# Performance work log

Measured on AMD Instinct MI355X. Metric: run time of the kernel, lower is better.

Reference implementation:

```python
import jax, jax.numpy as jnp
import numpy as np

INPUT_SIZE = 1024
OUTPUT_SIZE = 15
EXPERT_NUM = 10
BS = 65536


def setup_inputs() -> dict:
    key = jax.random.key(0)
    k1, k2, k3, k4, k5 = jax.random.split(key, 5)
    bound = 1.0 / np.sqrt(INPUT_SIZE)
    x = jax.random.normal(k1, (BS, INPUT_SIZE), dtype=jnp.float32)
    expert_w = jax.random.uniform(k2, (EXPERT_NUM, OUTPUT_SIZE, INPUT_SIZE), minval=-bound, maxval=bound, dtype=jnp.float32)
    expert_b = jax.random.uniform(k3, (EXPERT_NUM, OUTPUT_SIZE), minval=-bound, maxval=bound, dtype=jnp.float32)
    gate_w = jax.random.uniform(k4, (EXPERT_NUM, OUTPUT_SIZE, INPUT_SIZE), minval=-bound, maxval=bound, dtype=jnp.float32)
    gate_b = jax.random.uniform(k5, (EXPERT_NUM, OUTPUT_SIZE), minval=-bound, maxval=bound, dtype=jnp.float32)
    return {"x": x, "expert_w": expert_w, "expert_b": expert_b, "gate_w": gate_w, "gate_b": gate_b}


def reference(x, expert_w, expert_b, gate_w, gate_b):
    # miu, xi: (bs, out, E) -- matches torch.stack(..., dim=-1)
    miu = jnp.einsum('bi,eoi->boe', x, expert_w) + expert_b.T[None]  # (bs, out, E)
    xi = jnp.einsum('bi,eoi->boe', x, gate_w) + gate_b.T[None]       # (bs, out, E)
    g = jax.nn.softmax(xi, axis=-1)                                  # softmax over experts
    return jnp.sum(g * miu, axis=-1)                                 # (bs, out)
```

## Files before the change

### kernel.cpp

```cpp
#include <hip/hip_runtime.h>

#define KDIM 1024
#define NOUT 15
#define NEXP 10
#define BM   64
#define BK   32
#define NKS  32
#define QPT  20
#define SCOL 305

typedef short bf16x8 __attribute__((ext_vector_type(8)));
typedef float f32x16 __attribute__((ext_vector_type(16)));

__device__ __forceinline__ unsigned f2bf2(float a, float b) {
    unsigned ua = __float_as_uint(a);
    unsigned ub = __float_as_uint(b);
    ua = (ua + 0x7FFFu + ((ua >> 16) & 1u)) >> 16;
    ub = (ub + 0x7FFFu + ((ub >> 16) & 1u)) & 0xFFFF0000u;
    return ua | ub;
}

__device__ __forceinline__ void dma16(const void* g, void* l) {
    __builtin_amdgcn_global_load_lds(
        (const __attribute__((address_space(1))) unsigned int*)g,
        (__attribute__((address_space(3))) unsigned int*)l, 16, 0, 0);
}

__global__ void wconv_kernel(const float* __restrict__ ew,
                             const float* __restrict__ gw,
                             unsigned short* __restrict__ ws)
{
    int U  = blockIdx.x * 256 + threadIdx.x;
    int L  = U & 63;
    int q  = (U >> 6) % QPT;
    int ks = U / (QPT * 64);
    int nt = q >> 1, kt = q & 1;
    int wrow = nt * 32 + (L & 31);
    int wcol = ks * 32 + kt * 16 + (L >> 5) * 8;
    float4 a = {0.f,0.f,0.f,0.f}, b = {0.f,0.f,0.f,0.f};
    if (wrow < 150) {
        a = *(const float4*)(ew + wrow * KDIM + wcol);
        b = *(const float4*)(ew + wrow * KDIM + wcol + 4);
    } else if (wrow < 300) {
        a = *(const float4*)(gw + (wrow - 150) * KDIM + wcol);
        b = *(const float4*)(gw + (wrow - 150) * KDIM + wcol + 4);
    }
    uint4 o;
    o.x = f2bf2(a.x, a.y); o.y = f2bf2(a.z, a.w);
    o.z = f2bf2(b.x, b.y); o.w = f2bf2(b.z, b.w);
    *(uint4*)(ws + (size_t)U * 8) = o;
}

__global__ void __launch_bounds__(256, 3)
moe_kernel(const float* __restrict__ x,
           const unsigned short* __restrict__ wsrc,
           const float* __restrict__ eb,
           const float* __restrict__ gb,
           float* __restrict__ out)
{
    __shared__ union {
        unsigned short wb[2][QPT * 512];
        float ep[32][SCOL];
    } sm;

    const int tid = threadIdx.x;
    const int wv  = tid >> 6;
    const int L   = tid & 63;
    const int mw  = wv >> 1;
    const int nw  = wv & 1;
    const int ln  = L & 31;
    const int lh  = L >> 5;

    const float* xrow = x + ((size_t)blockIdx.x * BM + mw * 32 + ln) * KDIM + lh * 8;

    f32x16 acc[5];
    #pragma unroll
    for (int nt = 0; nt < 5; ++nt)
        #pragma unroll
        for (int r = 0; r < 16; ++r)
            acc[nt][r] = 0.f;

    #pragma unroll
    for (int i = 0; i < 5; ++i) {
        int q = wv * 5 + i;
        dma16(wsrc + ((size_t)q * 64 + L) * 8, &sm.wb[0][q * 512]);
    }
    float4 xa[2][2];
    #pragma unroll
    for (int kt = 0; kt < 2; ++kt) {
        xa[kt][0] = *(const float4*)(xrow + kt * 16);
        xa[kt][1] = *(const float4*)(xrow + kt * 16 + 4);
    }
    __syncthreads();

    #pragma unroll 2
    for (int ks = 0; ks < NKS; ++ks) {
        float4 xn[2][2];
        if (ks + 1 < NKS) {
            #pragma unroll
            for (int kt = 0; kt < 2; ++kt) {
                xn[kt][0] = *(const float4*)(xrow + (ks + 1) * 32 + kt * 16);
                xn[kt][1] = *(const float4*)(xrow + (ks + 1) * 32 + kt * 16 + 4);
            }
            #pragma unroll
            for (int i = 0; i < 5; ++i) {
                int q = wv * 5 + i;
                dma16(wsrc + (((size_t)(ks + 1) * QPT + q) * 64 + L) * 8,
                      &sm.wb[(ks + 1) & 1][q * 512]);
            }
        }

        bf16x8 af[2];
        #pragma unroll
        for (int kt = 0; kt < 2; ++kt) {
            union { unsigned u[4]; bf16x8 v; } pk;
            pk.u[0] = f2bf2(xa[kt][0].x, xa[kt][0].y);
            pk.u[1] = f2bf2(xa[kt][0].z, xa[kt][0].w);
            pk.u[2] = f2bf2(xa[kt][1].x, xa[kt][1].y);
            pk.u[3] = f2bf2(xa[kt][1].z, xa[kt][1].w);
            af[kt] = pk.v;
        }

        const unsigned short* wbuf = sm.wb[ks & 1];
        #pragma unroll
        for (int nt = 0; nt < 5; ++nt) {
            #pragma unroll
            for (int kt = 0; kt < 2; ++kt) {
                int q = (nw * 5 + nt) * 2 + kt;
                bf16x8 bf = *(const bf16x8*)&wbuf[q * 512 + L * 8];
                acc[nt] = __builtin_amdgcn_mfma_f32_32x32x16_bf16(af[kt], bf, acc[nt], 0, 0, 0);
            }
        }
        __syncthreads();

        #pragma unroll
        for (int kt = 0; kt < 2; ++kt) {
            xa[kt][0] = xn[kt][0];
            xa[kt][1] = xn[kt][1];
        }
    }

    #pragma unroll 1
    for (int g = 0; g < 2; ++g) {
        if (mw == g) {
            #pragma unroll
            for (int nt = 0; nt < 5; ++nt) {
                int col = nw * 160 + nt * 32 + ln;
                if (col < 300) {
                    #pragma unroll
                    for (int r = 0; r < 16; ++r)
                        sm.ep[(r & 3) + 8 * (r >> 2) + 4 * lh][col] = acc[nt][r];
                }
            }
        }
        __syncthreads();

        #pragma unroll 1
        for (int t = tid; t < 32 * NOUT; t += 256) {
            int row = t / NOUT, o = t % NOUT;
            float xi[NEXP], miu_v[NEXP];
            float mx = -1e30f;
            #pragma unroll
            for (int e = 0; e < NEXP; ++e) {
                miu_v[e] = sm.ep[row][e * NOUT + o]       + eb[e * NOUT + o];
                xi[e]    = sm.ep[row][150 + e * NOUT + o] + gb[e * NOUT + o];
                mx = fmaxf(mx, xi[e]);
            }
            float s = 0.f, v = 0.f;
            #pragma unroll
            for (int e = 0; e < NEXP; ++e) {
                float g2 = __expf(xi[e] - mx);
                s += g2;
                v += g2 * miu_v[e];
            }
            out[((size_t)blockIdx.x * BM + g * 32 + row) * NOUT + o] = v / s;
        }
        __syncthreads();
    }
}

extern "C" void kernel_launch(void* const* d_in, const int* in_sizes, int n_in,
                              void* d_out, int out_size, void* d_ws, size_t ws_size,
                              hipStream_t stream) {
    const float* x  = (const float*)d_in[0];
    const float* ew = (const float*)d_in[1];
    const float* eb = (const float*)d_in[2];
    const float* gw = (const float*)d_in[3];
    const float* gb = (const float*)d_in[4];
    float* out = (float*)d_out;
    unsigned short* ws = (unsigned short*)d_ws;

    wconv_kernel<<<160, 256, 0, stream>>>(ew, gw, ws);
    moe_kernel<<<65536 / BM, 256, 0, stream>>>(x, ws, eb, gb, out);
}
```

Before: 416.3 us.

## Stage x tile through LDS as bf16 to stop duplicate global loads

Before, each wave loaded its own copy of the x rows, so the two N-waves (nw=0,1) fetched and converted the same rows twice. Now the block loads each x element once with coalesced loads, converts it to bf16 and writes it into a double-buffered padded LDS tile. The MFMA fragments are then read back from LDS. The global prefetch distance also grows to two k-steps. This halves global x traffic and conversion work, but adds LDS writes and reads and raises shared memory use, which may reduce occupancy.

```diff
diff --git a/kernel.cpp b/kernel.cpp
--- a/kernel.cpp
+++ b/kernel.cpp
@@ -4,10 +4,10 @@
 #define NOUT 15
 #define NEXP 10
 #define BM   64
-#define BK   32
 #define NKS  32
 #define QPT  20
 #define SCOL 305
+#define XSTR 36
 
 typedef short bf16x8 __attribute__((ext_vector_type(8)));
 typedef float f32x16 __attribute__((ext_vector_type(16)));
@@ -59,7 +59,10 @@
            float* __restrict__ out)
 {
     __shared__ union {
-        unsigned short wb[2][QPT * 512];
+        struct {
+            unsigned short wb[2][QPT * 512];
+            unsigned short xb[2][64 * XSTR];
+        } k;
         float ep[32][SCOL];
     } sm;
 
@@ -71,7 +74,12 @@
     const int ln  = L & 31;
     const int lh  = L >> 5;
 
-    const float* xrow = x + ((size_t)blockIdx.x * BM + mw * 32 + ln) * KDIM + lh * 8;
+    const int srow = tid >> 2;
+    const int schk = tid & 3;
+    const float* xg = x + ((size_t)blockIdx.x * BM + srow) * KDIM + schk * 8;
+    const int xwo = srow * XSTR + schk * 8;
+
+    const int xfo = (mw * 32 + ln) * XSTR + lh * 8;
 
     f32x16 acc[5];
     #pragma unroll
@@ -83,61 +91,57 @@
     #pragma unroll
     for (int i = 0; i < 5; ++i) {
         int q = wv * 5 + i;
-        dma16(wsrc + ((size_t)q * 64 + L) * 8, &sm.wb[0][q * 512]);
+        dma16(wsrc + ((size_t)q * 64 + L) * 8, &sm.k.wb[0][q * 512]);
     }
-    float4 xa[2][2];
-    #pragma unroll
-    for (int kt = 0; kt < 2; ++kt) {
-        xa[kt][0] = *(const float4*)(xrow + kt * 16);
-        xa[kt][1] = *(const float4*)(xrow + kt * 16 + 4);
+    {
+        float4 a = *(const float4*)(xg);
+        float4 b = *(const float4*)(xg + 4);
+        uint4 o;
+        o.x = f2bf2(a.x, a.y); o.y = f2bf2(a.z, a.w);
+        o.z = f2bf2(b.x, b.y); o.w = f2bf2(b.z, b.w);
+        *(uint4*)&sm.k.xb[0][xwo] = o;
     }
+    float4 xa0 = *(const float4*)(xg + 32);
+    float4 xa1 = *(const float4*)(xg + 32 + 4);
     __syncthreads();
 
     #pragma unroll 2
     for (int ks = 0; ks < NKS; ++ks) {
-        float4 xn[2][2];
+        float4 xn0 = {0.f,0.f,0.f,0.f}, xn1 = {0.f,0.f,0.f,0.f};
+        if (ks + 2 < NKS) {
+            xn0 = *(const float4*)(xg + (ks + 2) * 32);
+            xn1 = *(const float4*)(xg + (ks + 2) * 32 + 4);
+        }
         if (ks + 1 < NKS) {
-            #pragma unroll
-            for (int kt = 0; kt < 2; ++kt) {
-                xn[kt][0] = *(const float4*)(xrow + (ks + 1) * 32 + kt * 16);
-                xn[kt][1] = *(const float4*)(xrow + (ks + 1) * 32 + kt * 16 + 4);
-            }
             #pragma unroll
             for (int i = 0; i < 5; ++i) {
                 int q = wv * 5 + i;
                 dma16(wsrc + (((size_t)(ks + 1) * QPT + q) * 64 + L) * 8,
-                      &sm.wb[(ks + 1) & 1][q * 512]);
+                      &sm.k.wb[(ks + 1) & 1][q * 512]);
             }
+            uint4 o;
+            o.x = f2bf2(xa0.x, xa0.y); o.y = f2bf2(xa0.z, xa0.w);
+            o.z = f2bf2(xa1.x, xa1.y); o.w = f2bf2(xa1.z, xa1.w);
+            *(uint4*)&sm.k.xb[(ks + 1) & 1][xwo] = o;
         }
 
-        bf16x8 af[2];
-        #pragma unroll
-        for (int kt = 0; kt < 2; ++kt) {
-            union { unsigned u[4]; bf16x8 v; } pk;
-            pk.u[0] = f2bf2(xa[kt][0].x, xa[kt][0].y);
-            pk.u[1] = f2bf2(xa[kt][0].z, xa[kt][0].w);
-            pk.u[2] = f2bf2(xa[kt][1].x, xa[kt][1].y);
-            pk.u[3] = f2bf2(xa[kt][1].z, xa[kt][1].w);
-            af[kt] = pk.v;
-        }
+        const unsigned short* xbuf = sm.k.xb[ks & 1];
+        bf16x8 af0 = *(const bf16x8*)&xbuf[xfo];
+        bf16x8 af1 = *(const bf16x8*)&xbuf[xfo + 16];
 
-        const unsigned short* wbuf = sm.wb[ks & 1];
+        const unsigned short* wbuf = sm.k.wb[ks & 1];
         #pragma unroll
         for (int nt = 0; nt < 5; ++nt) {
-            #pragma unroll
-            for (int kt = 0; kt < 2; ++kt) {
-                int q = (nw * 5 + nt) * 2 + kt;
-                bf16x8 bf = *(const bf16x8*)&wbuf[q * 512 + L * 8];
-                acc[nt] = __builtin_amdgcn_mfma_f32_32x32x16_bf16(af[kt], bf, acc[nt], 0, 0, 0);
-            }
+            int q = (nw * 5 + nt) * 2;
+            bf16x8 b0 = *(const bf16x8*)&wbuf[q * 512 + L * 8];
+            bf16x8 b1 = *(const bf16x8*)&wbuf[(q + 1) * 512 + L * 8];
+            acc[nt] = __builtin_amdgcn_mfma_f32_32x32x16_bf16(af0, b0, acc[nt], 0, 0, 0);
+            acc[nt] = __builtin_amdgcn_mfma_f32_32x32x16_bf16(af1, b1, acc[nt], 0, 0, 0);
         }
         __syncthreads();
 
-        #pragma unroll
-        for (int kt = 0; kt < 2; ++kt) {
-            xa[kt][0] = xn[kt][0];
-            xa[kt][1] = xn[kt][1];
-        }
+        xa0 = xn0;
+        xa1 = xn1;
     }
 
     #pragma unroll 1
```

After: 456.1 us. 9.6% more time.

## Double rows per block, reuse LDS weight fragments across two M tiles

Applied to the files above, without the earlier changes.

Raises the block tile from 64 to 128 rows so each wave computes two 32-row M tiles, and each weight fragment read from LDS feeds two MFMAs. This halves LDS traffic per MFMA. It also replaces __syncthreads with a custom barrier that waits only on the weight DMA (vmcnt(8)), so the next x loads can stay in flight across the barrier, and it moves the x prefetch directly into xa. Occupancy drops from 3 to 2 blocks per SM because the accumulators double, and the grid halves, which may reduce latency hiding.

```diff
diff --git a/kernel.cpp b/kernel.cpp
--- a/kernel.cpp
+++ b/kernel.cpp
@@ -3,8 +3,7 @@
 #define KDIM 1024
 #define NOUT 15
 #define NEXP 10
-#define BM   64
-#define BK   32
+#define BM   128
 #define NKS  32
 #define QPT  20
 #define SCOL 305
@@ -24,6 +23,13 @@
     __builtin_amdgcn_global_load_lds(
         (const __attribute__((address_space(1))) unsigned int*)g,
         (__attribute__((address_space(3))) unsigned int*)l, 16, 0, 0);
+}
+
+__device__ __forceinline__ void kbarrier() {
+    __builtin_amdgcn_sched_barrier(0);
+    asm volatile("s_waitcnt vmcnt(8) lgkmcnt(0)" ::: "memory");
+    __builtin_amdgcn_s_barrier();
+    __builtin_amdgcn_sched_barrier(0);
 }
 
 __global__ void wconv_kernel(const float* __restrict__ ew,
@@ -51,7 +57,7 @@
     *(uint4*)(ws + (size_t)U * 8) = o;
 }
 
-__global__ void __launch_bounds__(256, 3)
+__global__ void __launch_bounds__(256, 2)
 moe_kernel(const float* __restrict__ x,
            const unsigned short* __restrict__ wsrc,
            const float* __restrict__ eb,
@@ -71,37 +77,37 @@
     const int ln  = L & 31;
     const int lh  = L >> 5;
 
-    const float* xrow = x + ((size_t)blockIdx.x * BM + mw * 32 + ln) * KDIM + lh * 8;
-
-    f32x16 acc[5];
+    const float* xrow0 = x + ((size_t)blockIdx.x * BM + mw * 32 + ln) * KDIM + lh * 8;
+    const float* xrow1 = xrow0 + (size_t)64 * KDIM;
+
+    f32x16 acc[2][5];
     #pragma unroll
-    for (int nt = 0; nt < 5; ++nt)
+    for (int h = 0; h < 2; ++h)
         #pragma unroll
-        for (int r = 0; r < 16; ++r)
-            acc[nt][r] = 0.f;
+        for (int nt = 0; nt < 5; ++nt)
+            #pragma unroll
+            for (int r = 0; r < 16; ++r)
+                acc[h][nt][r] = 0.f;
 
     #pragma unroll
     for (int i = 0; i < 5; ++i) {
         int q = wv * 5 + i;
         dma16(wsrc + ((size_t)q * 64 + L) * 8, &sm.wb[0][q * 512]);
     }
-    float4 xa[2][2];
+    __builtin_amdgcn_sched_barrier(0);
+    float4 xa[2][2][2];
     #pragma unroll
     for (int kt = 0; kt < 2; ++kt) {
-        xa[kt][0] = *(const float4*)(xrow + kt * 16);
-        xa[kt][1] = *(const float4*)(xrow + kt * 16 + 4);
-    }
-    __syncthreads();
+        xa[0][kt][0] = *(const float4*)(xrow0 + kt * 16);
+        xa[0][kt][1] = *(const float4*)(xrow0 + kt * 16 + 4);
+        xa[1][kt][0] = *(const float4*)(xrow1 + kt * 16);
+        xa[1][kt][1] = *(const float4*)(xrow1 + kt * 16 + 4);
+    }
+    kbarrier();
 
     #pragma unroll 2
     for (int ks = 0; ks < NKS; ++ks) {
-        float4 xn[2][2];
         if (ks + 1 < NKS) {
-            #pragma unroll
-            for (int kt = 0; kt < 2; ++kt) {
-                xn[kt][0] = *(const float4*)(xrow + (ks + 1) * 32 + kt * 16);
-                xn[kt][1] = *(const float4*)(xrow + (ks + 1) * 32 + kt * 16 + 4);
-            }
             #pragma unroll
             for (int i = 0; i < 5; ++i) {
                 int q = wv * 5 + i;
@@ -109,47 +115,59 @@
                       &sm.wb[(ks + 1) & 1][q * 512]);
             }
         }
-
-        bf16x8 af[2];
+        __builtin_amdgcn_sched_barrier(0);
+
+        bf16x8 af[2][2];
         #pragma unroll
-        for (int kt = 0; kt < 2; ++kt) {
-            union { unsigned u[4]; bf16x8 v; } pk;
-            pk.u[0] = f2bf2(xa[kt][0].x, xa[kt][0].y);
-            pk.u[1] = f2bf2(xa[kt][0].z, xa[kt][0].w);
-            pk.u[2] = f2bf2(xa[kt][1].x, xa[kt][1].y);
-            pk.u[3] = f2bf2(xa[kt][1].z, xa[kt][1].w);
-            af[kt] = pk.v;
+        for (int h = 0; h < 2; ++h)
+            #pragma unroll
+            for (int kt = 0; kt < 2; ++kt) {
+                union { unsigned u[4]; bf16x8 v; } pk;
+                pk.u[0] = f2bf2(xa[h][kt][0].x, xa[h][kt][0].y);
+                pk.u[1] = f2bf2(xa[h][kt][0].z, xa[h][kt][0].w);
+                pk.u[2] = f2bf2(xa[h][kt][1].x, xa[h][kt][1].y);
+                pk.u[3] = f2bf2(xa[h][kt][1].z, xa[h][kt][1].w);
+                af[h][kt] = pk.v;
+            }
+
+        if (ks + 1 < NKS) {
+            #pragma unroll
+            for (int kt = 0; kt < 2; ++kt) {
+                xa[0][kt][0] = *(const float4*)(xrow0 + (ks + 1) * 32 + kt * 16);
+                xa[0][kt][1] = *(const float4*)(xrow0 + (ks + 1) * 32 + kt * 16 + 4);
+                xa[1][kt][0] = *(const float4*)(xrow1 + (ks + 1) * 32 + kt * 16);
+                xa[1][kt][1] = *(const float4*)(xrow1 + (ks + 1) * 32 + kt * 16 + 4);
+            }
         }
 
         const unsigned short* wbuf = sm.wb[ks & 1];
         #pragma unroll
         for (int nt = 0; nt < 5; ++nt) {
-            #pragma unroll
-            for (int kt = 0; kt < 2; ++kt) {
-                int q = (nw * 5 + nt) * 2 + kt;
-                bf16x8 bf = *(const bf16x8*)&wbuf[q * 512 + L * 8];
-                acc[nt] = __builtin_amdgcn_mfma_f32_32x32x16_bf16(af[kt], bf, acc[nt], 0, 0, 0);
-            }
-        }
-        __syncthreads();
-
-        #pragma unroll
-        for (int kt = 0; kt < 2; ++kt) {
-            xa[kt][0] = xn[kt][0];
-            xa[kt][1] = xn[kt][1];
-        }
-    }
+            int q = (nw * 5 + nt) * 2;
+            bf16x8 b0 = *(const bf16x8*)&wbuf[q * 512 + L * 8];
+            bf16x8 b1 = *(const bf16x8*)&wbuf[(q + 1) * 512 + L * 8];
+            acc[0][nt] = __builtin_amdgcn_mfma_f32_32x32x16_bf16(af[0][0], b0, acc[0][nt], 0, 0, 0);
+            acc[1][nt] = __builtin_amdgcn_mfma_f32_32x32x16_bf16(af[1][0], b0, acc[1][nt], 0, 0, 0);
+            acc[0][nt] = __builtin_amdgcn_mfma_f32_32x32x16_bf16(af[0][1], b1, acc[0][nt], 0, 0, 0);
+            acc[1][nt] = __builtin_amdgcn_mfma_f32_32x32x16_bf16(af[1][1], b1, acc[1][nt], 0, 0, 0);
+        }
+
+        kbarrier();
+    }
+
+    __syncthreads();
 
     #pragma unroll 1
-    for (int g = 0; g < 2; ++g) {
-        if (mw == g) {
+    for (int g = 0; g < 4; ++g) {
+        if (mw == (g & 1)) {
+            int h = g >> 1;
             #pragma unroll
             for (int nt = 0; nt < 5; ++nt) {
                 int col = nw * 160 + nt * 32 + ln;
                 if (col < 300) {
                     #pragma unroll
                     for (int r = 0; r < 16; ++r)
-                        sm.ep[(r & 3) + 8 * (r >> 2) + 4 * lh][col] = acc[nt][r];
+                        sm.ep[(r & 3) + 8 * (r >> 2) + 4 * lh][col] = acc[h][nt][r];
                 }
             }
         }
```

After: 451.6 us. 8.5% more time.
